# Kernel tuning notes

Measured on AMD Instinct MI355X. Metric: run time of the kernel, lower is better.

## Reference

```python
import jax, jax.numpy as jnp
import numpy as np

N = 100_000      # nodes
E = 1_600_000    # edges
DIN = 128
DH = 128
DOUT = 2
BN_EPS = 1e-5


def setup_inputs() -> dict:
    key = jax.random.key(0)
    ks = jax.random.split(key, 14)
    s_in = 1.0 / np.sqrt(DIN)
    s_h = 1.0 / np.sqrt(DH)
    return {
        "x": jax.random.normal(ks[0], (N, DIN), jnp.float32),
        "edge_index": jax.random.randint(ks[1], (2, E), 0, N, jnp.int32),
        "W1": jax.random.normal(ks[2], (DIN, DH), jnp.float32) * s_in,
        "b1": jnp.zeros((DH,), jnp.float32),
        "W2": jax.random.normal(ks[3], (DH, DH), jnp.float32) * s_h,
        "b2": jnp.zeros((DH,), jnp.float32),
        "W3": jax.random.normal(ks[4], (DH, DH), jnp.float32) * s_h,
        "b3": jnp.zeros((DH,), jnp.float32),
        "gamma": jnp.ones((DH,), jnp.float32),
        "beta": jnp.zeros((DH,), jnp.float32),
        "Wc": jax.random.normal(ks[5], (DH, DH), jnp.float32) * s_h,
        "bc": jnp.zeros((DH,), jnp.float32),
        "Wr": jax.random.normal(ks[6], (DH, DOUT), jnp.float32) * s_h,
        "br": jnp.zeros((DOUT,), jnp.float32),
    }


def reference(x, edge_index, W1, b1, W2, b2, W3, b3, gamma, beta, Wc, bc, Wr, br):
    src, dst = edge_index[0], edge_index[1]
    # GCN symmetric normalization with self-loops (deg includes self-loop)
    deg = jnp.zeros((N,), x.dtype).at[dst].add(1.0) + 1.0
    dinv = jax.lax.rsqrt(deg)
    coef = (dinv[src] * dinv[dst])[:, None]        # [E,1]
    self_coef = (dinv * dinv)[:, None]             # [N,1] self-loop weight

    def gcn_conv(h, W, b):
        h = h @ W                                  # [N,DH] dense transform
        agg = jnp.zeros((N, h.shape[1]), h.dtype).at[dst].add(h[src] * coef)
        return agg + h * self_coef + b

    h = jax.nn.relu(gcn_conv(x, W1, b1))
    h = jax.nn.relu(gcn_conv(h, W2, b2))   # dropout is identity at inference
    h = jax.nn.relu(gcn_conv(h, W3, b3))
    # BatchNorm1d over the node dimension (training-mode batch statistics)
    mu = h.mean(axis=0)
    var = h.var(axis=0)
    h = (h - mu) * jax.lax.rsqrt(var + BN_EPS) * gamma + beta
    h = jax.nn.relu(h @ Wc + bc)
    return h @ Wr + br
```

## Files before the change

kernel.cpp:

```cpp
#include <hip/hip_runtime.h>

#define DHC 128
#define BSHIFT 8
#define BSIZE 256

typedef __attribute__((ext_vector_type(8))) __bf16 bf16x8;
typedef __attribute__((ext_vector_type(8))) unsigned short ushort8;
typedef __attribute__((ext_vector_type(4))) float floatx4;

__device__ inline unsigned short f2bf(float f) {
    unsigned int u = __float_as_uint(f);
    return (unsigned short)((u + 0x7FFFu + ((u >> 16) & 1u)) >> 16);
}
__device__ inline float bf2f_lo(unsigned int v) { return __uint_as_float(v << 16); }
__device__ inline float bf2f_hi(unsigned int v) { return __uint_as_float(v & 0xFFFF0000u); }


__global__ __launch_bounds__(256) void bucket_hist(const int* __restrict__ dst,
                                                   int* __restrict__ bcount, int e, int eb,
                                                   const float* __restrict__ W1,
                                                   const float* __restrict__ W2,
                                                   const float* __restrict__ W3,
                                                   unsigned short* __restrict__ WTall,
                                                   unsigned short* __restrict__ dumA,
                                                   unsigned short* __restrict__ dumB) {
    if ((int)blockIdx.x >= eb) {
        int bb = (int)blockIdx.x - eb;
        if (bb == 0 && threadIdx.x < 128) {
            dumA[threadIdx.x] = 0;
            dumB[threadIdx.x] = 0;
        }
        int idx = bb * 256 + threadIdx.x;
        int wsel = idx >> 14;
        int i = idx & 16383;
        int nn = i >> 7, k = i & 127;
        const float* W = (wsel == 0) ? W1 : (wsel == 1) ? W2 : W3;
        WTall[idx] = f2bf(W[k * 128 + nn]);
        return;
    }
    __shared__ int h[512];
    for (int i = threadIdx.x; i < 512; i += 256) h[i] = 0;
    __syncthreads();
    int base = blockIdx.x * 4096 + threadIdx.x;
#pragma unroll
    for (int j = 0; j < 16; j++) {
        int i = base + j * 256;
        if (i < e) atomicAdd(&h[dst[i] >> BSHIFT], 1);
    }
    __syncthreads();
    for (int i = threadIdx.x; i < 512; i += 256)
        if (h[i]) atomicAdd(&bcount[i], h[i]);
}

__global__ void bucket_scan(const int* __restrict__ bcount, int* __restrict__ bbase,
                            int* __restrict__ bcur, int nb, int e) {
    __shared__ int s[512];
    int t = threadIdx.x;
    s[t] = (t < nb) ? bcount[t] : 0;
    __syncthreads();
    for (int off = 1; off < 512; off <<= 1) {
        int add = (t >= off) ? s[t - off] : 0;
        __syncthreads();
        s[t] += add;
        __syncthreads();
    }
    if (t < nb) {
        int ex = (t == 0) ? 0 : s[t - 1];
        bbase[t] = ex;
        bcur[t] = ex;
    }
    if (t == 0) bbase[nb] = e;
}

__global__ __launch_bounds__(256) void bucket_scatter(const int* __restrict__ src,
                                                      const int* __restrict__ dst,
                                                      int* __restrict__ bcur,
                                                      unsigned int* __restrict__ ebuf, int e) {
    __shared__ int h[512];
    __shared__ int rsv[512];
    for (int i = threadIdx.x; i < 512; i += 256) h[i] = 0;
    __syncthreads();
    int base = blockIdx.x * 4096 + threadIdx.x;
    int sreg[16], dreg[16];
#pragma unroll
    for (int j = 0; j < 16; j++) {
        int i = base + j * 256;
        if (i < e) {
            sreg[j] = src[i];
            dreg[j] = dst[i];
            atomicAdd(&h[dreg[j] >> BSHIFT], 1);
        } else {
            dreg[j] = -1;
        }
    }
    __syncthreads();
    for (int i = threadIdx.x; i < 512; i += 256) {
        int c = h[i];
        rsv[i] = c ? atomicAdd(&bcur[i], c) : 0;
        h[i] = 0;
    }
    __syncthreads();
#pragma unroll
    for (int j = 0; j < 16; j++) {
        if (dreg[j] >= 0) {
            int b = dreg[j] >> BSHIFT;
            int pos = rsv[b] + atomicAdd(&h[b], 1);
            ebuf[pos] = (unsigned int)sreg[j] | ((unsigned int)(dreg[j] & (BSIZE - 1)) << 20);
        }
    }
}

__global__ __launch_bounds__(256) void bucket_dega(const unsigned int* __restrict__ ebuf,
                                                   const int* __restrict__ bbase,
                                                   int* __restrict__ degs,
                                                   int* __restrict__ pbsum,
                                                   float* __restrict__ dinv, int n) {
    __shared__ int ldeg[256];
    __shared__ int red[256];
    int b = blockIdx.x, t = threadIdx.x;
    int beg = bbase[b], end = bbase[b + 1];
    ldeg[t] = 0;
    __syncthreads();
    for (int i = beg + t; i < end; i += 256) atomicAdd(&ldeg[ebuf[i] >> 20], 1);
    __syncthreads();
    int node = (b << BSHIFT) + t;
    int deg = ldeg[t];
    int pdeg = (deg + 7) & ~7;
    if (node < n) {
        degs[node] = deg;
        dinv[node] = rsqrtf((float)(deg + 1));
    } else {
        pdeg = 0;
    }
    red[t] = pdeg;
    __syncthreads();
    for (int off = 128; off > 0; off >>= 1) {
        if (t < off) red[t] += red[t + off];
        __syncthreads();
    }
    if (t == 0) pbsum[b] = red[0];
}

__global__ void pscan(const int* __restrict__ pbsum, int* __restrict__ pbase,
                      int* __restrict__ row_ptr, int nb, int n) {
    __shared__ int s[512];
    int t = threadIdx.x;
    s[t] = (t < nb) ? pbsum[t] : 0;
    __syncthreads();
    for (int off = 1; off < 512; off <<= 1) {
        int add = (t >= off) ? s[t - off] : 0;
        __syncthreads();
        s[t] += add;
        __syncthreads();
    }
    if (t < nb) pbase[t] = (t == 0) ? 0 : s[t - 1];
    if (t == 0) {
        pbase[nb] = s[nb - 1];
        row_ptr[n] = s[nb - 1];
    }
}

__global__ __launch_bounds__(256) void bucket_csr(const unsigned int* __restrict__ ebuf,
                                                  const int* __restrict__ bbase,
                                                  const int* __restrict__ pbase,
                                                  const int* __restrict__ degs,
                                                  int* __restrict__ row_ptr,
                                                  int* __restrict__ csr, int n) {
    __shared__ int lcur[256];
    __shared__ int lscan[256];
    int b = blockIdx.x, t = threadIdx.x;
    int beg = bbase[b], end = bbase[b + 1];
    int node = (b << BSHIFT) + t;
    int deg = (node < n) ? degs[node] : 0;
    int pdeg = (deg + 7) & ~7;
    lscan[t] = pdeg;
    __syncthreads();
    for (int off = 1; off < 256; off <<= 1) {
        int add = (t >= off) ? lscan[t - off] : 0;
        __syncthreads();
        lscan[t] += add;
        __syncthreads();
    }
    int rp = pbase[b] + lscan[t] - pdeg;
    if (node < n) row_ptr[node] = rp;
    lcur[t] = rp;
    __syncthreads();
    for (int i = beg + t; i < end; i += 256) {
        unsigned int p = ebuf[i];
        int pos = atomicAdd(&lcur[p >> 20], 1);
        csr[pos] = (int)(p & 0xFFFFFu);
    }
    __syncthreads();
    for (int j = deg; j < pdeg; j++) csr[rp + j] = n;
}

template <int MODE, int AF32>
__global__ __launch_bounds__(256, 4) void gemm_k(const void* __restrict__ Avoid,
                                                 const unsigned short* __restrict__ WT,
                                                 const float* __restrict__ bias,
                                                 const float* __restrict__ bias2,
                                                 unsigned short* __restrict__ outB,
                                                 float* __restrict__ outF,
                                                 const float* __restrict__ Wr,
                                                 const float* __restrict__ br,
                                                 const float* __restrict__ dinvp, int n) {
    __shared__ unsigned short Ws[32 * 512];
    {
        for (int c = threadIdx.x; c < 2048; c += 256) {
            int f = c >> 6;
            int l = c & 63;
            int ks = f >> 3, ct = f & 7;
            int nn = ct * 16 + (l & 15);
            int kb = ks * 32 + (l >> 4) * 8;
            *(uint4*)(&Ws[c * 8]) = *(const uint4*)(&WT[nn * 128 + kb]);
        }
    }
    __syncthreads();
    const int wave = threadIdx.x >> 6;
    const int lane = threadIdx.x & 63;
    const int rowbase = blockIdx.x * 128 + wave * 32;
    const int m = lane & 15;
    const int kq = lane >> 4;

    floatx4 acc[2][8];
#pragma unroll
    for (int rt = 0; rt < 2; rt++)
#pragma unroll
        for (int ct = 0; ct < 8; ct++) acc[rt][ct] = (floatx4){0.f, 0.f, 0.f, 0.f};

    const int r0 = min(rowbase + m, n - 1);
    const int r1 = min(rowbase + 16 + m, n - 1);

#pragma unroll
    for (int ks = 0; ks < 4; ks++) {
        const int kb = ks * 32 + kq * 8;
        bf16x8 a0, a1;
        if (AF32) {
            const float* Af = (const float*)Avoid;
            float4 f00 = *(const float4*)(Af + (size_t)r0 * 128 + kb);
            float4 f01 = *(const float4*)(Af + (size_t)r0 * 128 + kb + 4);
            float4 f10 = *(const float4*)(Af + (size_t)r1 * 128 + kb);
            float4 f11 = *(const float4*)(Af + (size_t)r1 * 128 + kb + 4);
            ushort8 u0, u1;
            u0[0] = f2bf(f00.x); u0[1] = f2bf(f00.y); u0[2] = f2bf(f00.z); u0[3] = f2bf(f00.w);
            u0[4] = f2bf(f01.x); u0[5] = f2bf(f01.y); u0[6] = f2bf(f01.z); u0[7] = f2bf(f01.w);
            u1[0] = f2bf(f10.x); u1[1] = f2bf(f10.y); u1[2] = f2bf(f10.z); u1[3] = f2bf(f10.w);
            u1[4] = f2bf(f11.x); u1[5] = f2bf(f11.y); u1[6] = f2bf(f11.z); u1[7] = f2bf(f11.w);
            a0 = __builtin_bit_cast(bf16x8, u0);
            a1 = __builtin_bit_cast(bf16x8, u1);
        } else {
            const unsigned short* Ab = (const unsigned short*)Avoid;
            a0 = __builtin_bit_cast(bf16x8, *(const ushort8*)(Ab + (size_t)r0 * 128 + kb));
            a1 = __builtin_bit_cast(bf16x8, *(const ushort8*)(Ab + (size_t)r1 * 128 + kb));
        }
#pragma unroll
        for (int ct = 0; ct < 8; ct++) {
            bf16x8 bfr = __builtin_bit_cast(bf16x8,
                *(const ushort8*)(&Ws[(ks * 8 + ct) * 512 + lane * 8]));
            acc[0][ct] = __builtin_amdgcn_mfma_f32_16x16x32_bf16(a0, bfr, acc[0][ct], 0, 0, 0);
            acc[1][ct] = __builtin_amdgcn_mfma_f32_16x16x32_bf16(a1, bfr, acc[1][ct], 0, 0, 0);
        }
    }

    if (MODE == 0) {
#pragma unroll
        for (int rt = 0; rt < 2; rt++) {
#pragma unroll
            for (int i = 0; i < 4; i++) {
                int r = rowbase + rt * 16 + kq * 4 + i;
                if (r < n) {
                    float dv = dinvp[r];
#pragma unroll
                    for (int ct = 0; ct < 8; ct++) {
                        int col = ct * 16 + m;
                        outB[(size_t)r * 128 + col] = f2bf(acc[rt][ct][i] * dv);
                    }
                }
            }
        }
    } else {
        float bcv[8], wr0[8], wr1[8];
#pragma unroll
        for (int ct = 0; ct < 8; ct++) {
            int col = ct * 16 + m;
            bcv[ct] = bias[col] + bias2[col];
            float2 wv = ((const float2*)Wr)[col];
            wr0[ct] = wv.x;
            wr1[ct] = wv.y;
        }
        float br0 = br[0], br1 = br[1];
#pragma unroll
        for (int rt = 0; rt < 2; rt++) {
#pragma unroll
            for (int i = 0; i < 4; i++) {
                float p0 = 0.f, p1 = 0.f;
#pragma unroll
                for (int ct = 0; ct < 8; ct++) {
                    float v = fmaxf(acc[rt][ct][i] + bcv[ct], 0.f);
                    p0 = fmaf(v, wr0[ct], p0);
                    p1 = fmaf(v, wr1[ct], p1);
                }
#pragma unroll
                for (int mk = 1; mk < 16; mk <<= 1) {
                    p0 += __shfl_xor(p0, mk);
                    p1 += __shfl_xor(p1, mk);
                }
                int r = rowbase + rt * 16 + kq * 4 + i;
                if (m == 0 && r < n) ((float2*)outF)[r] = make_float2(p0 + br0, p1 + br1);
            }
        }
    }
}

#define ACC8(v)                                          \
    a[0] += bf2f_lo((v).x); a[1] += bf2f_hi((v).x);      \
    a[2] += bf2f_lo((v).y); a[3] += bf2f_hi((v).y);      \
    a[4] += bf2f_lo((v).z); a[5] += bf2f_hi((v).z);      \
    a[6] += bf2f_lo((v).w); a[7] += bf2f_hi((v).w);

__global__ __launch_bounds__(256) void agg_k(const unsigned short* __restrict__ hS,
                                             const int* __restrict__ csr,
                                             const int* __restrict__ row_ptr,
                                             const float* __restrict__ dinv,
                                             const float* __restrict__ bias,
                                             unsigned short* __restrict__ out, int n) {
    int node = blockIdx.x * 16 + (threadIdx.x >> 4);
    int t = threadIdx.x & 15;
    if (node >= n) return;
    const uint4* h4 = (const uint4*)hS;
    uint4 vs = h4[(size_t)node * 16 + t];
    int beg = row_ptr[node], pend = row_ptr[node + 1];
    float dd = dinv[node];

    float a[8];
    a[0] = bf2f_lo(vs.x); a[1] = bf2f_hi(vs.x);
    a[2] = bf2f_lo(vs.y); a[3] = bf2f_hi(vs.y);
    a[4] = bf2f_lo(vs.z); a[5] = bf2f_hi(vs.z);
    a[6] = bf2f_lo(vs.w); a[7] = bf2f_hi(vs.w);

    const int4* cp = (const int4*)(csr + beg);
    int nc = (pend - beg) >> 3;
    if (nc > 0) {
        int4 i0 = cp[0], i1 = cp[1];
        for (int k = 0; k < nc; k++) {
            uint4 v0 = h4[(size_t)(unsigned)i0.x * 16 + t];
            uint4 v1 = h4[(size_t)(unsigned)i0.y * 16 + t];
            uint4 v2 = h4[(size_t)(unsigned)i0.z * 16 + t];
            uint4 v3 = h4[(size_t)(unsigned)i0.w * 16 + t];
            uint4 v4 = h4[(size_t)(unsigned)i1.x * 16 + t];
            uint4 v5 = h4[(size_t)(unsigned)i1.y * 16 + t];
            uint4 v6 = h4[(size_t)(unsigned)i1.z * 16 + t];
            uint4 v7 = h4[(size_t)(unsigned)i1.w * 16 + t];
            int4 p0 = cp[2 * k + 2];
            int4 p1 = cp[2 * k + 3];
            ACC8(v0); ACC8(v1); ACC8(v2); ACC8(v3);
            ACC8(v4); ACC8(v5); ACC8(v6); ACC8(v7);
            i0 = p0; i1 = p1;
        }
    }

    float4 b0 = ((const float4*)bias)[t * 2];
    float4 b1 = ((const float4*)bias)[t * 2 + 1];
    uint4 o;
    o.x = (unsigned int)f2bf(fmaxf(fmaf(dd, a[0], b0.x), 0.f)) |
          ((unsigned int)f2bf(fmaxf(fmaf(dd, a[1], b0.y), 0.f)) << 16);
    o.y = (unsigned int)f2bf(fmaxf(fmaf(dd, a[2], b0.z), 0.f)) |
          ((unsigned int)f2bf(fmaxf(fmaf(dd, a[3], b0.w), 0.f)) << 16);
    o.z = (unsigned int)f2bf(fmaxf(fmaf(dd, a[4], b1.x), 0.f)) |
          ((unsigned int)f2bf(fmaxf(fmaf(dd, a[5], b1.y), 0.f)) << 16);
    o.w = (unsigned int)f2bf(fmaxf(fmaf(dd, a[6], b1.z), 0.f)) |
          ((unsigned int)f2bf(fmaxf(fmaf(dd, a[7], b1.w), 0.f)) << 16);
    ((uint4*)out)[(size_t)node * 16 + t] = o;
}

__global__ __launch_bounds__(256) void bn_stats(const unsigned short* __restrict__ h,
                                                float* __restrict__ gsum,
                                                float* __restrict__ gsumsq, int n) {
    __shared__ float red[4][256];
    int l = threadIdx.x & 63;
    int rs = threadIdx.x >> 6;
    float s0 = 0.f, s1 = 0.f, q0 = 0.f, q1 = 0.f;
    for (int r = blockIdx.x * 4 + rs; r < n; r += gridDim.x * 4) {
        unsigned int v = *(const unsigned int*)(h + (size_t)r * 128 + l * 2);
        float a = bf2f_lo(v), b = bf2f_hi(v);
        s0 += a;
        s1 += b;
        q0 = fmaf(a, a, q0);
        q1 = fmaf(b, b, q1);
    }
    red[0][threadIdx.x] = s0;
    red[1][threadIdx.x] = s1;
    red[2][threadIdx.x] = q0;
    red[3][threadIdx.x] = q1;
    __syncthreads();
    if (threadIdx.x < 64) {
        float S0 = 0.f, S1 = 0.f, Q0 = 0.f, Q1 = 0.f;
#pragma unroll
        for (int j = 0; j < 4; j++) {
            S0 += red[0][j * 64 + l];
            S1 += red[1][j * 64 + l];
            Q0 += red[2][j * 64 + l];
            Q1 += red[3][j * 64 + l];
        }
        atomicAdd(&gsum[2 * l + 0], S0);
        atomicAdd(&gsum[2 * l + 1], S1);
        atomicAdd(&gsumsq[2 * l + 0], Q0);
        atomicAdd(&gsumsq[2 * l + 1], Q1);
    }
}

__global__ __launch_bounds__(256) void wcfold(const float* __restrict__ Wc,
                                              const float* __restrict__ gsum,
                                              const float* __restrict__ gsumsq,
                                              const float* __restrict__ gamma,
                                              const float* __restrict__ beta,
                                              unsigned short* __restrict__ WcT,
                                              float* __restrict__ bcP, float invN) {
    __shared__ float scS[128], shS[128];
    if (threadIdx.x < 128) {
        int j = threadIdx.x;
        float mu = gsum[j] * invN;
        float var = gsumsq[j] * invN - mu * mu;
        float sc = gamma[j] * rsqrtf(var + 1e-5f);
        scS[j] = sc;
        shS[j] = beta[j] - mu * sc;
    }
    __syncthreads();
    int idx = blockIdx.x * 256 + threadIdx.x;
    int j = idx & 127, k = idx >> 7;
    float w = Wc[k * 128 + j];
    WcT[j * 128 + k] = f2bf(scS[k] * w);
    atomicAdd(&bcP[j], shS[k] * w);
}


extern "C" void kernel_launch(void* const* d_in, const int* in_sizes, int n_in,
                              void* d_out, int out_size, void* d_ws, size_t ws_size,
                              hipStream_t stream) {
    const float* x = (const float*)d_in[0];
    const int* ei = (const int*)d_in[1];
    const float* W1 = (const float*)d_in[2];
    const float* b1 = (const float*)d_in[3];
    const float* W2 = (const float*)d_in[4];
    const float* b2 = (const float*)d_in[5];
    const float* W3 = (const float*)d_in[6];
    const float* b3 = (const float*)d_in[7];
    const float* gamma = (const float*)d_in[8];
    const float* beta = (const float*)d_in[9];
    const float* Wc = (const float*)d_in[10];
    const float* bc = (const float*)d_in[11];
    const float* Wr = (const float*)d_in[12];
    const float* br = (const float*)d_in[13];
    float* out = (float*)d_out;

    const int N = in_sizes[0] / DHC;
    const int E = in_sizes[1] / 2;
    const int* srcIdx = ei;
    const int* dstIdx = ei + E;
    const int NB = (N + BSIZE - 1) >> BSHIFT;

    char* w = (char*)d_ws;
    size_t off = 0;
    auto alloc = [&](size_t bytes) -> void* {
        void* p = w + off;
        off += (bytes + 255) & ~(size_t)255;
        return p;
    };
    unsigned short* bufA = (unsigned short*)alloc((size_t)(N + 1) * DHC * 2);
    unsigned short* bufB = (unsigned short*)alloc((size_t)(N + 1) * DHC * 2);
    unsigned int* ebuf = (unsigned int*)alloc((size_t)E * 4);
    int* csr_src = (int*)alloc(((size_t)E + 8 * (size_t)N + 16) * 4);
    int* row_ptr = (int*)alloc((size_t)(N + 1) * 4);
    float* dinv = (float*)alloc((size_t)N * 4);
    int* degs = (int*)alloc((size_t)N * 4);
    int* bcount = (int*)alloc(512 * 4 + 256 * 4 + 128 * 4);
    float* stats = (float*)(bcount + 512);
    float* gsum = stats;
    float* gsumsq = stats + 128;
    float* bcP = stats + 256;
    int* bbase = (int*)alloc(513 * 4);
    int* bcur = (int*)alloc(512 * 4);
    int* pbsum = (int*)alloc(512 * 4);
    int* pbase = (int*)alloc(513 * 4);
    unsigned short* WTall = (unsigned short*)alloc((size_t)3 * 16384 * 2);
    unsigned short* WT1 = WTall;
    unsigned short* WT2 = WTall + 16384;
    unsigned short* WT3 = WTall + 32768;
    unsigned short* WcT = (unsigned short*)alloc(16384 * 2);
    (void)ws_size; (void)n_in; (void)out_size;

    hipMemsetAsync(bcount, 0, 512 * 4 + 256 * 4 + 128 * 4, stream);

    const int EB = (E + 4095) / 4096;
    bucket_hist<<<EB + 192, 256, 0, stream>>>(dstIdx, bcount, E, EB, W1, W2, W3, WTall,
                                              bufA + (size_t)N * DHC, bufB + (size_t)N * DHC);
    bucket_scan<<<1, 512, 0, stream>>>(bcount, bbase, bcur, NB, E);
    bucket_scatter<<<EB, 256, 0, stream>>>(srcIdx, dstIdx, bcur, ebuf, E);
    bucket_dega<<<NB, 256, 0, stream>>>(ebuf, bbase, degs, pbsum, dinv, N);
    pscan<<<1, 512, 0, stream>>>(pbsum, pbase, row_ptr, NB, N);
    bucket_csr<<<NB, 256, 0, stream>>>(ebuf, bbase, pbase, degs, row_ptr, csr_src, N);

    const int gemmBlocks = (N + 127) / 128;
    const int aggBlocks = (N + 15) / 16;

    gemm_k<0, 1><<<gemmBlocks, 256, 0, stream>>>(x, WT1, nullptr, nullptr, bufB, nullptr, nullptr, nullptr, dinv, N);
    agg_k<<<aggBlocks, 256, 0, stream>>>(bufB, csr_src, row_ptr, dinv, b1, bufA, N);
    gemm_k<0, 0><<<gemmBlocks, 256, 0, stream>>>(bufA, WT2, nullptr, nullptr, bufB, nullptr, nullptr, nullptr, dinv, N);
    agg_k<<<aggBlocks, 256, 0, stream>>>(bufB, csr_src, row_ptr, dinv, b2, bufA, N);
    gemm_k<0, 0><<<gemmBlocks, 256, 0, stream>>>(bufA, WT3, nullptr, nullptr, bufB, nullptr, nullptr, nullptr, dinv, N);
    agg_k<<<aggBlocks, 256, 0, stream>>>(bufB, csr_src, row_ptr, dinv, b3, bufA, N);

    bn_stats<<<256, 256, 0, stream>>>(bufA, gsum, gsumsq, N);
    wcfold<<<64, 256, 0, stream>>>(Wc, gsum, gsumsq, gamma, beta, WcT, bcP, 1.0f / (float)N);
    gemm_k<2, 0><<<gemmBlocks, 256, 0, stream>>>(bufA, WcT, bcP, bc, nullptr, out, Wr, br, dinv, N);
}
```

Measured before the change: 444.5 us.

## Split aggregation by feature slices across blocks with nontemporal index loads and stores

New measurement: 868.7 us. +95.4%, slower.

```diff
diff --git a/kernel.cpp b/kernel.cpp
--- a/kernel.cpp
+++ b/kernel.cpp
@@ -7,6 +7,8 @@
 typedef __attribute__((ext_vector_type(8))) __bf16 bf16x8;
 typedef __attribute__((ext_vector_type(8))) unsigned short ushort8;
 typedef __attribute__((ext_vector_type(4))) float floatx4;
+typedef __attribute__((ext_vector_type(4))) int intx4;
+typedef __attribute__((ext_vector_type(4))) unsigned int uintx4;
 
 __device__ inline unsigned short f2bf(float f) {
     unsigned int u = __float_as_uint(f);
@@ -324,11 +326,12 @@
                                              const float* __restrict__ dinv,
                                              const float* __restrict__ bias,
                                              unsigned short* __restrict__ out, int n) {
-    int node = blockIdx.x * 16 + (threadIdx.x >> 4);
-    int t = threadIdx.x & 15;
+    const int slice = blockIdx.x & 7;
+    const int node = (blockIdx.x >> 3) * 128 + (threadIdx.x >> 1);
+    const int so = slice * 2 + (threadIdx.x & 1);
     if (node >= n) return;
     const uint4* h4 = (const uint4*)hS;
-    uint4 vs = h4[(size_t)node * 16 + t];
+    uint4 vs = h4[(size_t)node * 16 + so];
     int beg = row_ptr[node], pend = row_ptr[node + 1];
     float dd = dinv[node];
 
@@ -338,30 +341,26 @@
     a[4] = bf2f_lo(vs.z); a[5] = bf2f_hi(vs.z);
     a[6] = bf2f_lo(vs.w); a[7] = bf2f_hi(vs.w);
 
-    const int4* cp = (const int4*)(csr + beg);
+    const intx4* cp = (const intx4*)(csr + beg);
     int nc = (pend - beg) >> 3;
-    if (nc > 0) {
-        int4 i0 = cp[0], i1 = cp[1];
-        for (int k = 0; k < nc; k++) {
-            uint4 v0 = h4[(size_t)(unsigned)i0.x * 16 + t];
-            uint4 v1 = h4[(size_t)(unsigned)i0.y * 16 + t];
-            uint4 v2 = h4[(size_t)(unsigned)i0.z * 16 + t];
-            uint4 v3 = h4[(size_t)(unsigned)i0.w * 16 + t];
-            uint4 v4 = h4[(size_t)(unsigned)i1.x * 16 + t];
-            uint4 v5 = h4[(size_t)(unsigned)i1.y * 16 + t];
-            uint4 v6 = h4[(size_t)(unsigned)i1.z * 16 + t];
-            uint4 v7 = h4[(size_t)(unsigned)i1.w * 16 + t];
-            int4 p0 = cp[2 * k + 2];
-            int4 p1 = cp[2 * k + 3];
-            ACC8(v0); ACC8(v1); ACC8(v2); ACC8(v3);
-            ACC8(v4); ACC8(v5); ACC8(v6); ACC8(v7);
-            i0 = p0; i1 = p1;
-        }
-    }
-
-    float4 b0 = ((const float4*)bias)[t * 2];
-    float4 b1 = ((const float4*)bias)[t * 2 + 1];
-    uint4 o;
+    for (int k = 0; k < nc; k++) {
+        intx4 i0 = __builtin_nontemporal_load(cp + 2 * k);
+        intx4 i1 = __builtin_nontemporal_load(cp + 2 * k + 1);
+        uint4 v0 = h4[(size_t)(unsigned)i0.x * 16 + so];
+        uint4 v1 = h4[(size_t)(unsigned)i0.y * 16 + so];
+        uint4 v2 = h4[(size_t)(unsigned)i0.z * 16 + so];
+        uint4 v3 = h4[(size_t)(unsigned)i0.w * 16 + so];
+        uint4 v4 = h4[(size_t)(unsigned)i1.x * 16 + so];
+        uint4 v5 = h4[(size_t)(unsigned)i1.y * 16 + so];
+        uint4 v6 = h4[(size_t)(unsigned)i1.z * 16 + so];
+        uint4 v7 = h4[(size_t)(unsigned)i1.w * 16 + so];
+        ACC8(v0); ACC8(v1); ACC8(v2); ACC8(v3);
+        ACC8(v4); ACC8(v5); ACC8(v6); ACC8(v7);
+    }
+
+    float4 b0 = ((const float4*)bias)[so * 2];
+    float4 b1 = ((const float4*)bias)[so * 2 + 1];
+    uintx4 o;
     o.x = (unsigned int)f2bf(fmaxf(fmaf(dd, a[0], b0.x), 0.f)) |
           ((unsigned int)f2bf(fmaxf(fmaf(dd, a[1], b0.y), 0.f)) << 16);
     o.y = (unsigned int)f2bf(fmaxf(fmaf(dd, a[2], b0.z), 0.f)) |
@@ -370,7 +369,7 @@
           ((unsigned int)f2bf(fmaxf(fmaf(dd, a[5], b1.y), 0.f)) << 16);
     o.w = (unsigned int)f2bf(fmaxf(fmaf(dd, a[6], b1.z), 0.f)) |
           ((unsigned int)f2bf(fmaxf(fmaf(dd, a[7], b1.w), 0.f)) << 16);
-    ((uint4*)out)[(size_t)node * 16 + t] = o;
+    __builtin_nontemporal_store(o, (uintx4*)out + (size_t)node * 16 + so);
 }
 
 __global__ __launch_bounds__(256) void bn_stats(const unsigned short* __restrict__ h,
@@ -501,7 +500,7 @@
     bucket_csr<<<NB, 256, 0, stream>>>(ebuf, bbase, pbase, degs, row_ptr, csr_src, N);
 
     const int gemmBlocks = (N + 127) / 128;
-    const int aggBlocks = (N + 15) / 16;
+    const int aggBlocks = ((N + 127) / 128) * 8;
 
     gemm_k<0, 1><<<gemmBlocks, 256, 0, stream>>>(x, WT1, nullptr, nullptr, bufB, nullptr, nullptr, nullptr, dinv, N);
     agg_k<<<aggBlocks, 256, 0, stream>>>(bufB, csr_src, row_ptr, dinv, b1, bufA, N);
```
